# Kernel tuning notes

Measured on AMD Instinct MI355X. Metric: run time of the kernel, lower is better.

## Reference

```python
import jax, jax.numpy as jnp
import numpy as np

B, N, DIN, H, A = 4096, 32, 256, 128, 32  # batch, n_agents, din, hidden_dim, n_actions
NEG = 9e15


def _linear_params(key, fan_in, fan_out):
    kw, kb = jax.random.split(key)
    bound = 1.0 / np.sqrt(fan_in)
    w = jax.random.uniform(kw, (fan_in, fan_out), jnp.float32, -bound, bound)
    b = jax.random.uniform(kb, (fan_out,), jnp.float32, -bound, bound)
    return w, b


def setup_inputs() -> dict:
    key = jax.random.key(0)
    ks = jax.random.split(key, 12)
    x = jax.random.normal(ks[0], (B, N, DIN), jnp.float32)
    mask = jax.random.randint(ks[1], (B, N, N), 0, 2).astype(jnp.float32)
    enc_w, enc_b = _linear_params(ks[2], DIN, H)
    a1_vw, a1_vb = _linear_params(ks[3], H, H)
    a1_kw, a1_kb = _linear_params(ks[4], H, H)
    a1_qw, a1_qb = _linear_params(ks[5], H, H)
    a1_ow, a1_ob = _linear_params(ks[6], H, H)
    a2_vw, a2_vb = _linear_params(ks[7], H, H)
    a2_kw, a2_kb = _linear_params(ks[8], H, H)
    a2_qw, a2_qb = _linear_params(ks[9], H, H)
    a2_ow, a2_ob = _linear_params(ks[10], H, H)
    q_w, q_b = _linear_params(ks[11], H, A)
    return dict(x=x, mask=mask, enc_w=enc_w, enc_b=enc_b,
                a1_vw=a1_vw, a1_vb=a1_vb, a1_kw=a1_kw, a1_kb=a1_kb,
                a1_qw=a1_qw, a1_qb=a1_qb, a1_ow=a1_ow, a1_ob=a1_ob,
                a2_vw=a2_vw, a2_vb=a2_vb, a2_kw=a2_kw, a2_kb=a2_kb,
                a2_qw=a2_qw, a2_qb=a2_qb, a2_ow=a2_ow, a2_ob=a2_ob,
                q_w=q_w, q_b=q_b)


def _att_block(h, mask, vw, vb, kw, kb, qw, qb, ow, ob):
    # h: [B, N, H]; mask: [B, N, N]
    v = jax.nn.relu(jnp.einsum('bnd,dh->bnh', h, vw) + vb)
    q = jax.nn.relu(jnp.einsum('bnd,dh->bnh', h, qw) + qb)
    k = jax.nn.relu(jnp.einsum('bnd,dh->bnh', h, kw) + kb)
    scores = jnp.einsum('bih,bjh->bij', q, k)               # [B, N, N]
    logits = scores * mask - NEG * (1.0 - mask)
    att = jax.nn.softmax(logits, axis=2)
    out = jnp.einsum('bij,bjh->bih', att, v)
    return jax.nn.relu(jnp.einsum('bnh,ho->bno', out, ow) + ob)


def reference(x, mask, enc_w, enc_b,
              a1_vw, a1_vb, a1_kw, a1_kb, a1_qw, a1_qb, a1_ow, a1_ob,
              a2_vw, a2_vb, a2_kw, a2_kb, a2_qw, a2_qb, a2_ow, a2_ob,
              q_w, q_b):
    h1 = jax.nn.relu(jnp.einsum('bnd,dh->bnh', x, enc_w) + enc_b)
    h2 = _att_block(h1, mask, a1_vw, a1_vb, a1_kw, a1_kb, a1_qw, a1_qb, a1_ow, a1_ob)
    h3 = _att_block(h2, mask, a2_vw, a2_vb, a2_kw, a2_kb, a2_qw, a2_qb, a2_ow, a2_ob)
    q = jnp.einsum('bnh,ha->bna', h3, q_w) + q_b            # [B, N, A]
    return q
```

## Files before the change

kernel.cpp:

```cpp
#include <hip/hip_runtime.h>
#include <hip/hip_bf16.h>

typedef __attribute__((ext_vector_type(8))) short bf16x8;
typedef __attribute__((ext_vector_type(4))) short bf16x4;
typedef __attribute__((ext_vector_type(4))) float f32x4;

#define DEVI static __device__ __forceinline__

constexpr int NAG = 32, DIN = 256, HDIM = 128, ADIM = 32;
constexpr int G = 2;

constexpr int WS_ENC = 0;
constexpr int WS_H   = 32768;
constexpr int WS_QW  = 32768 + 8 * 16384;
constexpr int WS_TOT = WS_QW + 4096;

constexpr int L_R0 = 0;
constexpr int L_R1 = 17408;
constexpr int L_R2 = 34816;
constexpr int L_ST = 53248;
constexpr int L_TOT = 54272;

DEVI short f2bf(float f) {
  union { float f; unsigned u; } a; a.f = f;
  unsigned r = (a.u + 0x7fffu + ((a.u >> 16) & 1u)) >> 16;
  return (short)r;
}

__global__ void prep_weights(const float* __restrict__ enc_w,
                             const float* __restrict__ m0, const float* __restrict__ m1,
                             const float* __restrict__ m2, const float* __restrict__ m3,
                             const float* __restrict__ m4, const float* __restrict__ m5,
                             const float* __restrict__ m6, const float* __restrict__ m7,
                             const float* __restrict__ qw,
                             short* __restrict__ ws)
{
  const int i = blockIdx.x * 256 + threadIdx.x;
  if (i >= WS_TOT) return;
  const float* src; int Nout, e, base, sh, ntm;
  if (i < 32768) { src = enc_w; Nout = 128; e = i; base = 0; sh = 3; ntm = 7; }
  else if (i < WS_QW) {
    const int m = (i - 32768) >> 14;
    e = (i - 32768) & 16383; base = 32768 + (m << 14);
    const float* tab[8] = {m0, m1, m2, m3, m4, m5, m6, m7};
    src = tab[m]; Nout = 128; sh = 3; ntm = 7;
  } else { src = qw; Nout = 32; e = i - WS_QW; base = WS_QW; sh = 1; ntm = 1; }
  const int j = e & 7, lane = (e >> 3) & 63, tile = e >> 9;
  const int nt = tile & ntm, ks = tile >> sh;
  const int row = ks * 32 + (lane >> 4) * 8 + j;
  const int col = nt * 16 + (lane & 15);
  ws[base + e] = f2bf(src[row * Nout + col]);
}

template<int KSTEPS, bool RELU, bool TRANS>
DEVI void linearW(const short* __restrict__ src, int sstride,
                  const short* __restrict__ wfrag, const float* __restrict__ bias,
                  short* __restrict__ dst, int dstride,
                  int wave, int lr, int lq, int lane)
{
  f32x4 acc[4];
#pragma unroll
  for (int mt = 0; mt < 4; ++mt) acc[mt] = (f32x4){0.f, 0.f, 0.f, 0.f};

  const bf16x8* wp = (const bf16x8*)wfrag;
  bf16x8 bcur = wp[(0 * 8 + wave) * 64 + lane];
#pragma unroll
  for (int ks = 0; ks < KSTEPS; ++ks) {
    bf16x8 bnxt = bcur;
    if (ks + 1 < KSTEPS) bnxt = wp[((ks + 1) * 8 + wave) * 64 + lane];
    bf16x8 af[4];
#pragma unroll
    for (int mt = 0; mt < 4; ++mt)
      af[mt] = *(const bf16x8*)(src + (mt * 16 + lr) * sstride + ks * 32 + lq * 8);
#pragma unroll
    for (int mt = 0; mt < 4; ++mt)
      acc[mt] = __builtin_amdgcn_mfma_f32_16x16x32_bf16(af[mt], bcur, acc[mt], 0, 0, 0);
    bcur = bnxt;
  }

  const int col = wave * 16 + lr;
  const float bv = bias[col];
#pragma unroll
  for (int mt = 0; mt < 4; ++mt) {
    if (!TRANS) {
#pragma unroll
      for (int r = 0; r < 4; ++r) {
        float v = acc[mt][r] + bv;
        if (RELU) v = fmaxf(v, 0.f);
        dst[(mt * 16 + lq * 4 + r) * dstride + col] = f2bf(v);
      }
    } else {
      bf16x4 s;
#pragma unroll
      for (int r = 0; r < 4; ++r) {
        float v = acc[mt][r] + bv;
        if (RELU) v = fmaxf(v, 0.f);
        s[r] = f2bf(v);
      }
      *(bf16x4*)(dst + col * dstride + mt * 16 + lq * 4) = s;
    }
  }
}

DEVI void att_block(short* Rh, short* Rq, short* R2, float* ST,
                    const short* wv, const short* wk, const short* wq, const short* wo,
                    const float* bv, const float* bk, const float* bq, const float* bo,
                    const float* __restrict__ mask, int b0,
                    int wave, int lr, int lq, int lane)
{
  linearW<4, true, false>(Rh, 136, wq, bq, Rq, 136, wave, lr, lq, lane);
  linearW<4, true, false>(Rh, 136, wk, bk, R2, 136, wave, lr, lq, lane);
  __syncthreads();

  const int g = wave >> 2, smt = (wave >> 1) & 1, snt = wave & 1;
  float lg[4];
  {
    f32x4 sacc = (f32x4){0, 0, 0, 0};
#pragma unroll
    for (int ks = 0; ks < 4; ++ks) {
      const bf16x8 qf = *(const bf16x8*)(Rq + (g * 32 + smt * 16 + lr) * 136 + ks * 32 + lq * 8);
      const bf16x8 kf = *(const bf16x8*)(R2 + (g * 32 + snt * 16 + lr) * 136 + ks * 32 + lq * 8);
      sacc = __builtin_amdgcn_mfma_f32_16x16x32_bf16(qf, kf, sacc, 0, 0, 0);
    }
    const float* mp = mask + (size_t)(b0 + g) * (NAG * NAG);
#pragma unroll
    for (int r = 0; r < 4; ++r) {
      const int row = smt * 16 + lq * 4 + r, col = snt * 16 + lr;
      const float m = mp[row * 32 + col];
      const float l = sacc[r] * m - 9e15f * (1.f - m);
      lg[r] = l;
      float v = l;
      v = fmaxf(v, __shfl_xor(v, 1)); v = fmaxf(v, __shfl_xor(v, 2));
      v = fmaxf(v, __shfl_xor(v, 4)); v = fmaxf(v, __shfl_xor(v, 8));
      float e = __expf(l - v);
      e += __shfl_xor(e, 1); e += __shfl_xor(e, 2);
      e += __shfl_xor(e, 4); e += __shfl_xor(e, 8);
      if (lr == 0) {
        float2 p; p.x = v; p.y = e;
        *(float2*)(ST + (g * 32 + row) * 4 + snt * 2) = p;
      }
    }
  }
  __syncthreads();

  short* AT = Rq;
#pragma unroll
  for (int r = 0; r < 4; ++r) {
    const int row = g * 32 + smt * 16 + lq * 4 + r, col = snt * 16 + lr;
    const float4 s4 = *(const float4*)(ST + row * 4);
    const float M = fmaxf(s4.x, s4.z);
    const float T = s4.y * __expf(s4.x - M) + s4.w * __expf(s4.z - M);
    const float a = __expf(lg[r] - M) / T;
    AT[row * 40 + col] = f2bf(a);
  }

  linearW<4, true, true>(Rh, 136, wv, bv, R2, 72, wave, lr, lq, lane);
  __syncthreads();

  {
    const int cq = wave & 3, pg = wave >> 2;
    f32x4 acc[2][2];
#pragma unroll
    for (int mt = 0; mt < 2; ++mt)
#pragma unroll
      for (int nt = 0; nt < 2; ++nt) acc[mt][nt] = (f32x4){0, 0, 0, 0};
    bf16x8 pa[2];
#pragma unroll
    for (int mt = 0; mt < 2; ++mt)
      pa[mt] = *(const bf16x8*)(AT + (pg * 32 + mt * 16 + lr) * 40 + lq * 8);
#pragma unroll
    for (int nt = 0; nt < 2; ++nt) {
      const bf16x8 vf = *(const bf16x8*)(R2 + (cq * 32 + nt * 16 + lr) * 72 + pg * 32 + lq * 8);
#pragma unroll
      for (int mt = 0; mt < 2; ++mt)
        acc[mt][nt] = __builtin_amdgcn_mfma_f32_16x16x32_bf16(pa[mt], vf, acc[mt][nt], 0, 0, 0);
    }
#pragma unroll
    for (int nt = 0; nt < 2; ++nt)
#pragma unroll
      for (int mt = 0; mt < 2; ++mt)
#pragma unroll
        for (int r = 0; r < 4; ++r) {
          const int row = pg * 32 + mt * 16 + lq * 4 + r;
          const int col = cq * 32 + nt * 16 + lr;
          Rh[row * 136 + col] = f2bf(acc[mt][nt][r]);
        }
  }
  __syncthreads();

  linearW<4, true, false>(Rh, 136, wo, bo, Rq, 136, wave, lr, lq, lane);
  __syncthreads();
}

__global__ __launch_bounds__(512, 6)
void dgn_main(const float* __restrict__ x, const float* __restrict__ mask,
              const float* __restrict__ enc_b,
              const float* __restrict__ b1v, const float* __restrict__ b1k,
              const float* __restrict__ b1q, const float* __restrict__ b1o,
              const float* __restrict__ b2v, const float* __restrict__ b2k,
              const float* __restrict__ b2q, const float* __restrict__ b2o,
              const float* __restrict__ qb,
              const short* __restrict__ wf,
              float* __restrict__ out)
{
  __shared__ __align__(16) char smem[L_TOT];
  short* R0 = (short*)(smem + L_R0);
  short* R1 = (short*)(smem + L_R1);
  short* R2 = (short*)(smem + L_R2);
  float* ST = (float*)(smem + L_ST);
  short* XB = (short*)(smem + L_R1);

  const int tid = threadIdx.x;
  const int wave = tid >> 6, lane = tid & 63;
  const int lr = lane & 15, lq = lane >> 4;
  const int b0 = blockIdx.x * G;

  {
    const float4* xsrc = (const float4*)(x + (size_t)b0 * NAG * DIN);
#pragma unroll
    for (int it = 0; it < 8; ++it) {
      const int q4 = tid + it * 512;
      const float4 v = xsrc[q4];
      const int row = q4 >> 6;
      const int col = (q4 & 63) * 4;
      bf16x4 s;
      s[0] = f2bf(v.x); s[1] = f2bf(v.y); s[2] = f2bf(v.z); s[3] = f2bf(v.w);
      *(bf16x4*)(XB + row * 264 + col) = s;
    }
  }
  __syncthreads();

  linearW<8, true, false>(XB, 264, wf + WS_ENC, enc_b, R0, 136, wave, lr, lq, lane);
  __syncthreads();

  att_block(R0, R1, R2, ST,
            wf + WS_H + 0 * 16384, wf + WS_H + 1 * 16384,
            wf + WS_H + 2 * 16384, wf + WS_H + 3 * 16384,
            b1v, b1k, b1q, b1o, mask, b0, wave, lr, lq, lane);

  att_block(R1, R0, R2, ST,
            wf + WS_H + 4 * 16384, wf + WS_H + 5 * 16384,
            wf + WS_H + 6 * 16384, wf + WS_H + 7 * 16384,
            b2v, b2k, b2q, b2o, mask, b0, wave, lr, lq, lane);

  {
    const int hmt = wave >> 1, ht = wave & 1;
    f32x4 facc = (f32x4){0, 0, 0, 0};
    const bf16x8* wp = (const bf16x8*)(wf + WS_QW);
    bf16x8 bq[4];
#pragma unroll
    for (int ks = 0; ks < 4; ++ks)
      bq[ks] = wp[(ks * 2 + ht) * 64 + lane];
#pragma unroll
    for (int ks = 0; ks < 4; ++ks) {
      const bf16x8 af = *(const bf16x8*)(R0 + (hmt * 16 + lr) * 136 + ks * 32 + lq * 8);
      facc = __builtin_amdgcn_mfma_f32_16x16x32_bf16(af, bq[ks], facc, 0, 0, 0);
    }
    const int col = ht * 16 + lr;
    const float bvv = qb[col];
#pragma unroll
    for (int r = 0; r < 4; ++r) {
      const int row = hmt * 16 + lq * 4 + r;
      const int gg = row >> 5, ag = row & 31;
      out[(((size_t)(b0 + gg) * NAG) + ag) * ADIM + col] = facc[r] + bvv;
    }
  }
}

extern "C" void kernel_launch(void* const* d_in, const int* in_sizes, int n_in,
                              void* d_out, int out_size, void* d_ws, size_t ws_size,
                              hipStream_t stream)
{
  const float* x     = (const float*)d_in[0];
  const float* mask  = (const float*)d_in[1];
  const float* enc_w = (const float*)d_in[2];
  const float* enc_b = (const float*)d_in[3];
  const float* a1_vw = (const float*)d_in[4];
  const float* a1_vb = (const float*)d_in[5];
  const float* a1_kw = (const float*)d_in[6];
  const float* a1_kb = (const float*)d_in[7];
  const float* a1_qw = (const float*)d_in[8];
  const float* a1_qb = (const float*)d_in[9];
  const float* a1_ow = (const float*)d_in[10];
  const float* a1_ob = (const float*)d_in[11];
  const float* a2_vw = (const float*)d_in[12];
  const float* a2_vb = (const float*)d_in[13];
  const float* a2_kw = (const float*)d_in[14];
  const float* a2_kb = (const float*)d_in[15];
  const float* a2_qw = (const float*)d_in[16];
  const float* a2_qb = (const float*)d_in[17];
  const float* a2_ow = (const float*)d_in[18];
  const float* a2_ob = (const float*)d_in[19];
  const float* q_w   = (const float*)d_in[20];
  const float* q_b   = (const float*)d_in[21];
  short* ws = (short*)d_ws;

  prep_weights<<<(WS_TOT + 255) / 256, 256, 0, stream>>>(
      enc_w, a1_vw, a1_kw, a1_qw, a1_ow, a2_vw, a2_kw, a2_qw, a2_ow, q_w, ws);

  dgn_main<<<4096 / G, 512, 0, stream>>>(
      x, mask, enc_b,
      a1_vb, a1_kb, a1_qb, a1_ob,
      a2_vb, a2_kb, a2_qb, a2_ob,
      q_b, ws, (float*)d_out);
}
```

Baseline: 320.6 us.

## Fuse QKV projections, swap MFMA operands, and single-pass softmax per wave

Restructures the attention block so one pass computes Q, K and V together, sharing the hidden-state fragment loads. It also swaps the MFMA operand roles so outputs can be stored as vectors with float4 bias loads. Softmax now runs in one pass inside each wave, removing the cross-wave statistics buffer and one barrier. V and the attention matrix get their own LDS regions, and the weight prep kernel is vectorised. In exchange, LDS use grows and launch bounds drop to 4 blocks per CU, so occupancy is lower and half the waves sit idle during the scores and final-projection stages.

```diff
diff --git a/kernel.cpp b/kernel.cpp
--- a/kernel.cpp
+++ b/kernel.cpp
@@ -15,16 +15,21 @@
 constexpr int WS_QW  = 32768 + 8 * 16384;
 constexpr int WS_TOT = WS_QW + 4096;
 
+constexpr int SH = 136;
+constexpr int SV = 72;
+constexpr int SA = 40;
+constexpr int SX = 264;
+
 constexpr int L_R0 = 0;
 constexpr int L_R1 = 17408;
 constexpr int L_R2 = 34816;
-constexpr int L_ST = 53248;
-constexpr int L_TOT = 54272;
+constexpr int L_RV = 52224;
+constexpr int L_AT = 70656;
+constexpr int L_TOT = 75776;
 
 DEVI short f2bf(float f) {
   union { float f; unsigned u; } a; a.f = f;
-  unsigned r = (a.u + 0x7fffu + ((a.u >> 16) & 1u)) >> 16;
-  return (short)r;
+  return (short)((a.u + 0x7fffu + ((a.u >> 16) & 1u)) >> 16);
 }
 
 __global__ void prep_weights(const float* __restrict__ enc_w,
@@ -35,164 +40,241 @@
                              const float* __restrict__ qw,
                              short* __restrict__ ws)
 {
-  const int i = blockIdx.x * 256 + threadIdx.x;
-  if (i >= WS_TOT) return;
-  const float* src; int Nout, e, base, sh, ntm;
-  if (i < 32768) { src = enc_w; Nout = 128; e = i; base = 0; sh = 3; ntm = 7; }
-  else if (i < WS_QW) {
-    const int m = (i - 32768) >> 14;
-    e = (i - 32768) & 16383; base = 32768 + (m << 14);
-    const float* tab[8] = {m0, m1, m2, m3, m4, m5, m6, m7};
-    src = tab[m]; Nout = 128; sh = 3; ntm = 7;
-  } else { src = qw; Nout = 32; e = i - WS_QW; base = WS_QW; sh = 1; ntm = 1; }
-  const int j = e & 7, lane = (e >> 3) & 63, tile = e >> 9;
-  const int nt = tile & ntm, ks = tile >> sh;
-  const int row = ks * 32 + (lane >> 4) * 8 + j;
-  const int col = nt * 16 + (lane & 15);
-  ws[base + e] = f2bf(src[row * Nout + col]);
-}
-
-template<int KSTEPS, bool RELU, bool TRANS>
-DEVI void linearW(const short* __restrict__ src, int sstride,
-                  const short* __restrict__ wfrag, const float* __restrict__ bias,
-                  short* __restrict__ dst, int dstride,
-                  int wave, int lr, int lq, int lane)
-{
-  f32x4 acc[4];
-#pragma unroll
-  for (int mt = 0; mt < 4; ++mt) acc[mt] = (f32x4){0.f, 0.f, 0.f, 0.f};
+  const int blk = blockIdx.x, tid = threadIdx.x;
+  const float* src; int base, NM, nsh, f4;
+  if (blk < 32) { src = enc_w; base = WS_ENC; NM = 8; nsh = 7; f4 = blk * 256 + tid; }
+  else if (blk < 160) {
+    const int m = (blk - 32) >> 4;
+    if      (m == 0) src = m0; else if (m == 1) src = m1;
+    else if (m == 2) src = m2; else if (m == 3) src = m3;
+    else if (m == 4) src = m4; else if (m == 5) src = m5;
+    else if (m == 6) src = m6; else             src = m7;
+    base = WS_H + (m << 14); NM = 8; nsh = 7; f4 = ((blk - 32) & 15) * 256 + tid;
+  } else { src = qw; base = WS_QW; NM = 2; nsh = 5; f4 = (blk - 160) * 256 + tid; }
+  const int s = f4 * 4;
+  const int row = s >> nsh, col0 = s & ((1 << nsh) - 1);
+  const float4 v = *(const float4*)(src + s);
+  const int j = row & 7, ks = row >> 5, lhi = ((row >> 3) & 3) * 16;
+  const float vv[4] = {v.x, v.y, v.z, v.w};
+#pragma unroll
+  for (int c = 0; c < 4; ++c) {
+    const int col = col0 + c;
+    const int mt = col >> 4, lane = lhi + (col & 15);
+    ws[base + (((ks * NM + mt) * 64 + lane) << 3) + j] = f2bf(vv[c]);
+  }
+}
+
+template<int KSTEPS, bool RELU>
+DEVI void linearSw(const short* __restrict__ src, int sstride,
+                   const short* __restrict__ wfrag, const float* __restrict__ bias,
+                   short* __restrict__ dst,
+                   int wave, int lr, int lq, int lane)
+{
+  const int mg = wave >> 1, ng = wave & 1;
+  f32x4 acc[2][2];
+#pragma unroll
+  for (int a = 0; a < 2; ++a)
+#pragma unroll
+    for (int b = 0; b < 2; ++b) acc[a][b] = (f32x4){0.f, 0.f, 0.f, 0.f};
 
   const bf16x8* wp = (const bf16x8*)wfrag;
-  bf16x8 bcur = wp[(0 * 8 + wave) * 64 + lane];
 #pragma unroll
   for (int ks = 0; ks < KSTEPS; ++ks) {
-    bf16x8 bnxt = bcur;
-    if (ks + 1 < KSTEPS) bnxt = wp[((ks + 1) * 8 + wave) * 64 + lane];
-    bf16x8 af[4];
-#pragma unroll
-    for (int mt = 0; mt < 4; ++mt)
-      af[mt] = *(const bf16x8*)(src + (mt * 16 + lr) * sstride + ks * 32 + lq * 8);
-#pragma unroll
-    for (int mt = 0; mt < 4; ++mt)
-      acc[mt] = __builtin_amdgcn_mfma_f32_16x16x32_bf16(af[mt], bcur, acc[mt], 0, 0, 0);
-    bcur = bnxt;
-  }
-
-  const int col = wave * 16 + lr;
-  const float bv = bias[col];
-#pragma unroll
-  for (int mt = 0; mt < 4; ++mt) {
-    if (!TRANS) {
+    bf16x8 hb[2];
+#pragma unroll
+    for (int b = 0; b < 2; ++b)
+      hb[b] = *(const bf16x8*)(src + ((ng * 2 + b) * 16 + lr) * sstride + ks * 32 + lq * 8);
+    bf16x8 wa[2];
+#pragma unroll
+    for (int a = 0; a < 2; ++a)
+      wa[a] = wp[(ks * 8 + mg * 2 + a) * 64 + lane];
+#pragma unroll
+    for (int a = 0; a < 2; ++a)
+#pragma unroll
+      for (int b = 0; b < 2; ++b)
+        acc[a][b] = __builtin_amdgcn_mfma_f32_16x16x32_bf16(wa[a], hb[b], acc[a][b], 0, 0, 0);
+  }
+#pragma unroll
+  for (int a = 0; a < 2; ++a) {
+    const float4 bv = *(const float4*)(bias + (mg * 2 + a) * 16 + lq * 4);
+    const float bb[4] = {bv.x, bv.y, bv.z, bv.w};
+#pragma unroll
+    for (int b = 0; b < 2; ++b) {
+      bf16x4 s;
 #pragma unroll
       for (int r = 0; r < 4; ++r) {
-        float v = acc[mt][r] + bv;
-        if (RELU) v = fmaxf(v, 0.f);
-        dst[(mt * 16 + lq * 4 + r) * dstride + col] = f2bf(v);
-      }
-    } else {
-      bf16x4 s;
-#pragma unroll
-      for (int r = 0; r < 4; ++r) {
-        float v = acc[mt][r] + bv;
+        float v = acc[a][b][r] + bb[r];
         if (RELU) v = fmaxf(v, 0.f);
         s[r] = f2bf(v);
       }
-      *(bf16x4*)(dst + col * dstride + mt * 16 + lq * 4) = s;
-    }
-  }
-}
-
-DEVI void att_block(short* Rh, short* Rq, short* R2, float* ST,
+      *(bf16x4*)(dst + ((ng * 2 + b) * 16 + lr) * SH + (mg * 2 + a) * 16 + lq * 4) = s;
+    }
+  }
+}
+
+DEVI void qkv_pass(const short* __restrict__ h,
+                   const short* __restrict__ wq, const short* __restrict__ wk,
+                   const short* __restrict__ wv,
+                   const float* __restrict__ bq, const float* __restrict__ bk,
+                   const float* __restrict__ bv,
+                   short* __restrict__ Q, short* __restrict__ K, short* __restrict__ V,
+                   int wave, int lr, int lq, int lane)
+{
+  const int mg = wave >> 1, ng = wave & 1;
+  f32x4 qa[2][2], ka[2][2], va[2][2];
+#pragma unroll
+  for (int a = 0; a < 2; ++a)
+#pragma unroll
+    for (int b = 0; b < 2; ++b) {
+      qa[a][b] = (f32x4){0.f, 0.f, 0.f, 0.f};
+      ka[a][b] = (f32x4){0.f, 0.f, 0.f, 0.f};
+      va[a][b] = (f32x4){0.f, 0.f, 0.f, 0.f};
+    }
+  const bf16x8* wpq = (const bf16x8*)wq;
+  const bf16x8* wpk = (const bf16x8*)wk;
+  const bf16x8* wpv = (const bf16x8*)wv;
+#pragma unroll
+  for (int ks = 0; ks < 4; ++ks) {
+    bf16x8 hf[2];
+#pragma unroll
+    for (int b = 0; b < 2; ++b)
+      hf[b] = *(const bf16x8*)(h + ((ng * 2 + b) * 16 + lr) * SH + ks * 32 + lq * 8);
+#pragma unroll
+    for (int a = 0; a < 2; ++a) {
+      const bf16x8 wqf = wpq[(ks * 8 + mg * 2 + a) * 64 + lane];
+      const bf16x8 wkf = wpk[(ks * 8 + mg * 2 + a) * 64 + lane];
+      const bf16x8 wvf = wpv[(ks * 8 + mg * 2 + a) * 64 + lane];
+#pragma unroll
+      for (int b = 0; b < 2; ++b) {
+        qa[a][b] = __builtin_amdgcn_mfma_f32_16x16x32_bf16(wqf, hf[b], qa[a][b], 0, 0, 0);
+        ka[a][b] = __builtin_amdgcn_mfma_f32_16x16x32_bf16(wkf, hf[b], ka[a][b], 0, 0, 0);
+        va[b][a] = __builtin_amdgcn_mfma_f32_16x16x32_bf16(hf[b], wvf, va[b][a], 0, 0, 0);
+      }
+    }
+  }
+#pragma unroll
+  for (int a = 0; a < 2; ++a) {
+    const float4 bq4 = *(const float4*)(bq + (mg * 2 + a) * 16 + lq * 4);
+    const float4 bk4 = *(const float4*)(bk + (mg * 2 + a) * 16 + lq * 4);
+    const float qb4[4] = {bq4.x, bq4.y, bq4.z, bq4.w};
+    const float kb4[4] = {bk4.x, bk4.y, bk4.z, bk4.w};
+#pragma unroll
+    for (int b = 0; b < 2; ++b) {
+      bf16x4 sq, sk;
+#pragma unroll
+      for (int r = 0; r < 4; ++r) {
+        sq[r] = f2bf(fmaxf(qa[a][b][r] + qb4[r], 0.f));
+        sk[r] = f2bf(fmaxf(ka[a][b][r] + kb4[r], 0.f));
+      }
+      const int off = ((ng * 2 + b) * 16 + lr) * SH + (mg * 2 + a) * 16 + lq * 4;
+      *(bf16x4*)(Q + off) = sq;
+      *(bf16x4*)(K + off) = sk;
+    }
+  }
+#pragma unroll
+  for (int a = 0; a < 2; ++a) {
+    const float bvv = bv[(mg * 2 + a) * 16 + lr];
+#pragma unroll
+    for (int b = 0; b < 2; ++b) {
+      bf16x4 sv;
+#pragma unroll
+      for (int r = 0; r < 4; ++r)
+        sv[r] = f2bf(fmaxf(va[b][a][r] + bvv, 0.f));
+      *(bf16x4*)(V + ((mg * 2 + a) * 16 + lr) * SV + (ng * 2 + b) * 16 + lq * 4) = sv;
+    }
+  }
+}
+
+DEVI void scores_pass(const short* __restrict__ Q, const short* __restrict__ K,
+                      short* __restrict__ AT, const float* __restrict__ mask, int b0,
+                      int wave, int lr, int lq, int lane)
+{
+  const int g = wave >> 1, qt = wave & 1;
+  f32x4 sc[2];
+  sc[0] = (f32x4){0.f, 0.f, 0.f, 0.f};
+  sc[1] = (f32x4){0.f, 0.f, 0.f, 0.f};
+#pragma unroll
+  for (int ks = 0; ks < 4; ++ks) {
+    const bf16x8 qf = *(const bf16x8*)(Q + (g * 32 + qt * 16 + lr) * SH + ks * 32 + lq * 8);
+#pragma unroll
+    for (int kt = 0; kt < 2; ++kt) {
+      const bf16x8 kf = *(const bf16x8*)(K + (g * 32 + kt * 16 + lr) * SH + ks * 32 + lq * 8);
+      sc[kt] = __builtin_amdgcn_mfma_f32_16x16x32_bf16(kf, qf, sc[kt], 0, 0, 0);
+    }
+  }
+  const float* mp = mask + (size_t)(b0 + g) * (NAG * NAG) + (qt * 16 + lr) * 32;
+  float l[2][4];
+  float M = -3.0e38f;
+#pragma unroll
+  for (int kt = 0; kt < 2; ++kt) {
+    const float4 m4 = *(const float4*)(mp + kt * 16 + lq * 4);
+    const float mm[4] = {m4.x, m4.y, m4.z, m4.w};
+#pragma unroll
+    for (int r = 0; r < 4; ++r) {
+      const float v = sc[kt][r] * mm[r] - 9e15f * (1.f - mm[r]);
+      l[kt][r] = v;
+      M = fmaxf(M, v);
+    }
+  }
+  M = fmaxf(M, __shfl_xor(M, 16));
+  M = fmaxf(M, __shfl_xor(M, 32));
+  float e[2][4], T = 0.f;
+#pragma unroll
+  for (int kt = 0; kt < 2; ++kt)
+#pragma unroll
+    for (int r = 0; r < 4; ++r) { e[kt][r] = __expf(l[kt][r] - M); T += e[kt][r]; }
+  T += __shfl_xor(T, 16);
+  T += __shfl_xor(T, 32);
+  const float rT = __frcp_rn(T);
+#pragma unroll
+  for (int kt = 0; kt < 2; ++kt) {
+    bf16x4 s;
+#pragma unroll
+    for (int r = 0; r < 4; ++r) s[r] = f2bf(e[kt][r] * rT);
+    *(bf16x4*)(AT + (g * 32 + qt * 16 + lr) * SA + kt * 16 + lq * 4) = s;
+  }
+}
+
+DEVI void pv_pass(const short* __restrict__ V, const short* __restrict__ AT,
+                  short* __restrict__ AO, int wave, int lr, int lq, int lane)
+{
+  const int g = wave >> 2, qt = (wave >> 1) & 1, fh = wave & 1;
+  const bf16x8 atf = *(const bf16x8*)(AT + (g * 32 + qt * 16 + lr) * SA + lq * 8);
+  f32x4 pacc[4];
+#pragma unroll
+  for (int f = 0; f < 4; ++f) {
+    const int ft = fh * 4 + f;
+    const bf16x8 vf = *(const bf16x8*)(V + (ft * 16 + lr) * SV + g * 32 + lq * 8);
+    pacc[f] = __builtin_amdgcn_mfma_f32_16x16x32_bf16(
+        vf, atf, (f32x4){0.f, 0.f, 0.f, 0.f}, 0, 0, 0);
+  }
+#pragma unroll
+  for (int f = 0; f < 4; ++f) {
+    const int ft = fh * 4 + f;
+    bf16x4 s;
+#pragma unroll
+    for (int r = 0; r < 4; ++r) s[r] = f2bf(pacc[f][r]);
+    *(bf16x4*)(AO + (g * 32 + qt * 16 + lr) * SH + ft * 16 + lq * 4) = s;
+  }
+}
+
+DEVI void att_block(short* Rh, short* Rq, short* RK, short* RV_, short* ATb,
                     const short* wv, const short* wk, const short* wq, const short* wo,
                     const float* bv, const float* bk, const float* bq, const float* bo,
                     const float* __restrict__ mask, int b0,
                     int wave, int lr, int lq, int lane)
 {
-  linearW<4, true, false>(Rh, 136, wq, bq, Rq, 136, wave, lr, lq, lane);
-  linearW<4, true, false>(Rh, 136, wk, bk, R2, 136, wave, lr, lq, lane);
-  __syncthreads();
-
-  const int g = wave >> 2, smt = (wave >> 1) & 1, snt = wave & 1;
-  float lg[4];
-  {
-    f32x4 sacc = (f32x4){0, 0, 0, 0};
-#pragma unroll
-    for (int ks = 0; ks < 4; ++ks) {
-      const bf16x8 qf = *(const bf16x8*)(Rq + (g * 32 + smt * 16 + lr) * 136 + ks * 32 + lq * 8);
-      const bf16x8 kf = *(const bf16x8*)(R2 + (g * 32 + snt * 16 + lr) * 136 + ks * 32 + lq * 8);
-      sacc = __builtin_amdgcn_mfma_f32_16x16x32_bf16(qf, kf, sacc, 0, 0, 0);
-    }
-    const float* mp = mask + (size_t)(b0 + g) * (NAG * NAG);
-#pragma unroll
-    for (int r = 0; r < 4; ++r) {
-      const int row = smt * 16 + lq * 4 + r, col = snt * 16 + lr;
-      const float m = mp[row * 32 + col];
-      const float l = sacc[r] * m - 9e15f * (1.f - m);
-      lg[r] = l;
-      float v = l;
-      v = fmaxf(v, __shfl_xor(v, 1)); v = fmaxf(v, __shfl_xor(v, 2));
-      v = fmaxf(v, __shfl_xor(v, 4)); v = fmaxf(v, __shfl_xor(v, 8));
-      float e = __expf(l - v);
-      e += __shfl_xor(e, 1); e += __shfl_xor(e, 2);
-      e += __shfl_xor(e, 4); e += __shfl_xor(e, 8);
-      if (lr == 0) {
-        float2 p; p.x = v; p.y = e;
-        *(float2*)(ST + (g * 32 + row) * 4 + snt * 2) = p;
-      }
-    }
-  }
-  __syncthreads();
-
-  short* AT = Rq;
-#pragma unroll
-  for (int r = 0; r < 4; ++r) {
-    const int row = g * 32 + smt * 16 + lq * 4 + r, col = snt * 16 + lr;
-    const float4 s4 = *(const float4*)(ST + row * 4);
-    const float M = fmaxf(s4.x, s4.z);
-    const float T = s4.y * __expf(s4.x - M) + s4.w * __expf(s4.z - M);
-    const float a = __expf(lg[r] - M) / T;
-    AT[row * 40 + col] = f2bf(a);
-  }
-
-  linearW<4, true, true>(Rh, 136, wv, bv, R2, 72, wave, lr, lq, lane);
-  __syncthreads();
-
-  {
-    const int cq = wave & 3, pg = wave >> 2;
-    f32x4 acc[2][2];
-#pragma unroll
-    for (int mt = 0; mt < 2; ++mt)
-#pragma unroll
-      for (int nt = 0; nt < 2; ++nt) acc[mt][nt] = (f32x4){0, 0, 0, 0};
-    bf16x8 pa[2];
-#pragma unroll
-    for (int mt = 0; mt < 2; ++mt)
-      pa[mt] = *(const bf16x8*)(AT + (pg * 32 + mt * 16 + lr) * 40 + lq * 8);
-#pragma unroll
-    for (int nt = 0; nt < 2; ++nt) {
-      const bf16x8 vf = *(const bf16x8*)(R2 + (cq * 32 + nt * 16 + lr) * 72 + pg * 32 + lq * 8);
-#pragma unroll
-      for (int mt = 0; mt < 2; ++mt)
-        acc[mt][nt] = __builtin_amdgcn_mfma_f32_16x16x32_bf16(pa[mt], vf, acc[mt][nt], 0, 0, 0);
-    }
-#pragma unroll
-    for (int nt = 0; nt < 2; ++nt)
-#pragma unroll
-      for (int mt = 0; mt < 2; ++mt)
-#pragma unroll
-        for (int r = 0; r < 4; ++r) {
-          const int row = pg * 32 + mt * 16 + lq * 4 + r;
-          const int col = cq * 32 + nt * 16 + lr;
-          Rh[row * 136 + col] = f2bf(acc[mt][nt][r]);
-        }
-  }
-  __syncthreads();
-
-  linearW<4, true, false>(Rh, 136, wo, bo, Rq, 136, wave, lr, lq, lane);
-  __syncthreads();
-}
-
-__global__ __launch_bounds__(512, 6)
+  qkv_pass(Rh, wq, wk, wv, bq, bk, bv, Rq, RK, RV_, wave, lr, lq, lane);
+  __syncthreads();
+  if (wave < 4) scores_pass(Rq, RK, ATb, mask, b0, wave, lr, lq, lane);
+  __syncthreads();
+  pv_pass(RV_, ATb, Rh, wave, lr, lq, lane);
+  __syncthreads();
+  linearSw<4, true>(Rh, SH, wo, bo, Rq, wave, lr, lq, lane);
+  __syncthreads();
+}
+
+__global__ __launch_bounds__(512, 4)
 void dgn_main(const float* __restrict__ x, const float* __restrict__ mask,
               const float* __restrict__ enc_b,
               const float* __restrict__ b1v, const float* __restrict__ b1k,
@@ -207,7 +289,8 @@
   short* R0 = (short*)(smem + L_R0);
   short* R1 = (short*)(smem + L_R1);
   short* R2 = (short*)(smem + L_R2);
-  float* ST = (float*)(smem + L_ST);
+  short* RV_ = (short*)(smem + L_RV);
+  short* ATb = (short*)(smem + L_AT);
   short* XB = (short*)(smem + L_R1);
 
   const int tid = threadIdx.x;
@@ -221,48 +304,47 @@
     for (int it = 0; it < 8; ++it) {
       const int q4 = tid + it * 512;
       const float4 v = xsrc[q4];
-      const int row = q4 >> 6;
-      const int col = (q4 & 63) * 4;
       bf16x4 s;
       s[0] = f2bf(v.x); s[1] = f2bf(v.y); s[2] = f2bf(v.z); s[3] = f2bf(v.w);
-      *(bf16x4*)(XB + row * 264 + col) = s;
-    }
-  }
-  __syncthreads();
-
-  linearW<8, true, false>(XB, 264, wf + WS_ENC, enc_b, R0, 136, wave, lr, lq, lane);
-  __syncthreads();
-
-  att_block(R0, R1, R2, ST,
+      *(bf16x4*)(XB + (q4 >> 6) * SX + (q4 & 63) * 4) = s;
+    }
+  }
+  __syncthreads();
+
+  linearSw<8, true>(XB, SX, wf + WS_ENC, enc_b, R0, wave, lr, lq, lane);
+  __syncthreads();
+
+  att_block(R0, R1, R2, RV_, ATb,
             wf + WS_H + 0 * 16384, wf + WS_H + 1 * 16384,
             wf + WS_H + 2 * 16384, wf + WS_H + 3 * 16384,
             b1v, b1k, b1q, b1o, mask, b0, wave, lr, lq, lane);
 
-  att_block(R1, R0, R2, ST,
+  att_block(R1, R0, R2, RV_, ATb,
             wf + WS_H + 4 * 16384, wf + WS_H + 5 * 16384,
             wf + WS_H + 6 * 16384, wf + WS_H + 7 * 16384,
             b2v, b2k, b2q, b2o, mask, b0, wave, lr, lq, lane);
 
-  {
-    const int hmt = wave >> 1, ht = wave & 1;
-    f32x4 facc = (f32x4){0, 0, 0, 0};
+  if (wave < 4) {
+    f32x4 ha[2];
+    ha[0] = (f32x4){0.f, 0.f, 0.f, 0.f};
+    ha[1] = (f32x4){0.f, 0.f, 0.f, 0.f};
     const bf16x8* wp = (const bf16x8*)(wf + WS_QW);
-    bf16x8 bq[4];
-#pragma unroll
-    for (int ks = 0; ks < 4; ++ks)
-      bq[ks] = wp[(ks * 2 + ht) * 64 + lane];
 #pragma unroll
     for (int ks = 0; ks < 4; ++ks) {
-      const bf16x8 af = *(const bf16x8*)(R0 + (hmt * 16 + lr) * 136 + ks * 32 + lq * 8);
-      facc = __builtin_amdgcn_mfma_f32_16x16x32_bf16(af, bq[ks], facc, 0, 0, 0);
-    }
-    const int col = ht * 16 + lr;
-    const float bvv = qb[col];
-#pragma unroll
-    for (int r = 0; r < 4; ++r) {
-      const int row = hmt * 16 + lq * 4 + r;
-      const int gg = row >> 5, ag = row & 31;
-      out[(((size_t)(b0 + gg) * NAG) + ag) * ADIM + col] = facc[r] + bvv;
+      const bf16x8 hf = *(const bf16x8*)(R0 + (wave * 16 + lr) * SH + ks * 32 + lq * 8);
+#pragma unroll
+      for (int a = 0; a < 2; ++a)
+        ha[a] = __builtin_amdgcn_mfma_f32_16x16x32_bf16(wp[(ks * 2 + a) * 64 + lane], hf, ha[a], 0, 0, 0);
+    }
+    const int row = wave * 16 + lr;
+    float* op = out + (((size_t)(b0 + (row >> 5)) * NAG) + (row & 31)) * ADIM;
+#pragma unroll
+    for (int a = 0; a < 2; ++a) {
+      const float4 bv4 = *(const float4*)(qb + a * 16 + lq * 4);
+      float4 o;
+      o.x = ha[a][0] + bv4.x; o.y = ha[a][1] + bv4.y;
+      o.z = ha[a][2] + bv4.z; o.w = ha[a][3] + bv4.w;
+      *(float4*)(op + a * 16 + lq * 4) = o;
     }
   }
 }
@@ -295,7 +377,7 @@
   const float* q_b   = (const float*)d_in[21];
   short* ws = (short*)d_ws;
 
-  prep_weights<<<(WS_TOT + 255) / 256, 256, 0, stream>>>(
+  prep_weights<<<164, 256, 0, stream>>>(
       enc_w, a1_vw, a1_kw, a1_qw, a1_ow, a2_vw, a2_kw, a2_qw, a2_ow, q_w, ws);
 
   dgn_main<<<4096 / G, 512, 0, stream>>>(
```

Result: faster. 313.2 us (-2.3%).
